# Kernel optimization log

Measured on AMD Instinct MI355X. Metric: run time of the kernel, lower is better.

The kernel has to match this reference:

```python
import jax, jax.numpy as jnp
import numpy as np

B, T, C = 4, 2048, 1024
H = 16
D = C // H  # 64


def setup_inputs() -> dict:
    key = jax.random.key(0)
    ks = jax.random.split(key, 5)
    scale = 0.02
    x = jax.random.normal(ks[0], (B, T, C), dtype=jnp.float32)
    # Linear weights stored in [in, out] layout (equivalent to torch W.T)
    W_qkv = jax.random.normal(ks[1], (C, 3 * C), dtype=jnp.float32) * scale
    b_qkv = jax.random.normal(ks[2], (3 * C,), dtype=jnp.float32) * scale
    W_out = jax.random.normal(ks[3], (C, C), dtype=jnp.float32) * scale
    b_out = jax.random.normal(ks[4], (C,), dtype=jnp.float32) * scale
    return {"x": x, "W_qkv": W_qkv, "b_qkv": b_qkv, "W_out": W_out, "b_out": b_out}


def reference(x, W_qkv, b_qkv, W_out, b_out):
    Bx, Tx, Cx = x.shape
    qkv = x @ W_qkv + b_qkv                      # [B,T,3C]
    qkv = qkv.reshape(Bx, Tx, 3, H, D)
    q = jnp.transpose(qkv[:, :, 0], (0, 2, 1, 3))  # [B,H,T,D]
    k = jnp.transpose(qkv[:, :, 1], (0, 2, 1, 3))
    v = jnp.transpose(qkv[:, :, 2], (0, 2, 1, 3))
    scores = jnp.einsum('bhqd,bhkd->bhqk', q, k) / jnp.sqrt(jnp.float32(D))
    causal = jnp.tril(jnp.ones((Tx, Tx), dtype=bool))  # keep lower triangle
    scores = jnp.where(causal, scores, jnp.float32(-jnp.inf))
    w = jax.nn.softmax(scores, axis=-1)           # dropout p=0.0 (eval)
    out = jnp.einsum('bhqk,bhkd->bhqd', w, v)     # [B,H,T,D]
    out = jnp.transpose(out, (0, 2, 1, 3)).reshape(Bx, Tx, Cx)
    return out @ W_out + b_out
```

## Files before the change

kernel.cpp:

```cpp
#include <hip/hip_runtime.h>

typedef _Float16 f16;
typedef _Float16 f16x4 __attribute__((ext_vector_type(4)));
typedef _Float16 f16x8 __attribute__((ext_vector_type(8)));
typedef float    f32x4 __attribute__((ext_vector_type(4)));

#define B_ 4
#define T_ 2048
#define C_ 1024
#define H_ 16
#define D_ 64

__device__ __forceinline__ void gload_lds16(const f16* g, f16* l) {
  __builtin_amdgcn_global_load_lds(
      (const __attribute__((address_space(1))) unsigned int*)g,
      (__attribute__((address_space(3))) unsigned int*)l, 16, 0, 0);
}

__global__ void cvt_kernel(const float* __restrict__ in, f16* __restrict__ out, int n4) {
  int i = blockIdx.x * blockDim.x + threadIdx.x;
  int stride = gridDim.x * blockDim.x;
  for (; i < n4; i += stride) {
    float4 v = ((const float4*)in)[i];
    f16x4 h = { (f16)v.x, (f16)v.y, (f16)v.z, (f16)v.w };
    ((f16x4*)out)[i] = h;
  }
}

__global__ void transpose_cvt_kernel(const float* __restrict__ W, f16* __restrict__ Wt,
                                     int K, int N) {
  __shared__ f16 tile[32][33];
  int bx = blockIdx.x, by = blockIdx.y;
  int tx = threadIdx.x & 31, ty = threadIdx.x >> 5;
  #pragma unroll
  for (int i = ty; i < 32; i += 8)
    tile[i][tx] = (f16)W[(size_t)(by * 32 + i) * N + bx * 32 + tx];
  __syncthreads();
  #pragma unroll
  for (int i = ty; i < 32; i += 8)
    Wt[(size_t)(bx * 32 + i) * K + by * 32 + tx] = tile[tx][i];
}

template <int EPI>
__global__ __launch_bounds__(256, 3)
void gemm_kernel(const f16* __restrict__ A, const f16* __restrict__ Bt,
                 const float* __restrict__ bias, float* __restrict__ outF,
                 f16* __restrict__ q, f16* __restrict__ kk, f16* __restrict__ vt,
                 int M, int N, int K) {
  __shared__ __align__(16) f16 As[3][128 * 32];
  __shared__ __align__(16) f16 Bs[3][128 * 32];
  const int nbn = N >> 7;
  const int bid = blockIdx.x;
  const int bm = bid / nbn, bn = bid % nbn;
  const int m0 = bm << 7, n0 = bn << 7;
  const int tid = threadIdx.x;
  const int lane = tid & 63, wid = tid >> 6;
  const int wr = wid >> 1, wc = wid & 1;

  f32x4 acc[4][4] = {};

  const int srow = lane >> 2;
  const int scol = (((lane & 3) ^ ((lane >> 2) & 3)) << 3);
  const f16* Abase = A + (size_t)(m0 + srow) * K + scol;
  const f16* Bbase = Bt + (size_t)(n0 + srow) * K + scol;

  auto stage = [&](int buf, int kt) {
    const int c0 = wid * 2;
    #pragma unroll
    for (int c = c0; c < c0 + 2; ++c) {
      gload_lds16(Abase + (size_t)c * 16 * K + kt * 32, &As[buf][c * 512]);
      gload_lds16(Bbase + (size_t)c * 16 * K + kt * 32, &Bs[buf][c * 512]);
    }
  };

  const int g = lane >> 4;
  const int rr = lane & 15;
  const int swz = (g ^ (rr & 3)) << 4;

  auto compute = [&](int buf) {
    f16x8 af[4], bf[4];
    #pragma unroll
    for (int t = 0; t < 4; ++t) {
      af[t] = *(const f16x8*)((const char*)&As[buf][0] + (wr * 64 + t * 16 + rr) * 64 + swz);
      bf[t] = *(const f16x8*)((const char*)&Bs[buf][0] + (wc * 64 + t * 16 + rr) * 64 + swz);
    }
    __builtin_amdgcn_s_setprio(1);
    #pragma unroll
    for (int i = 0; i < 4; ++i)
      #pragma unroll
      for (int j = 0; j < 4; ++j)
        acc[i][j] = __builtin_amdgcn_mfma_f32_16x16x32_f16(af[i], bf[j], acc[i][j], 0, 0, 0);
    __builtin_amdgcn_s_setprio(0);
  };

  const int nk = K >> 5;
  int bcur = 0, bnext = 1, bnn = 2;
  stage(0, 0);
  stage(1, 1);
  asm volatile("s_waitcnt vmcnt(4)" ::: "memory");
  __builtin_amdgcn_s_barrier();
  __builtin_amdgcn_sched_barrier(0);
  for (int t = 0; t < nk; ++t) {
    if (t + 2 < nk) stage(bnn, t + 2);
    compute(bcur);
    if (t + 1 < nk) {
      if (t + 2 < nk) asm volatile("s_waitcnt vmcnt(4)" ::: "memory");
      else            asm volatile("s_waitcnt vmcnt(0)" ::: "memory");
      __builtin_amdgcn_s_barrier();
      __builtin_amdgcn_sched_barrier(0);
    }
    const int tmp = bcur; bcur = bnext; bnext = bnn; bnn = tmp;
  }

  const int col = lane & 15;
  const int row4 = (lane >> 4) << 2;
  #pragma unroll
  for (int i = 0; i < 4; ++i) {
    #pragma unroll
    for (int j = 0; j < 4; ++j) {
      const int n = n0 + wc * 64 + j * 16 + col;
      const float bn_ = bias[n];
      #pragma unroll
      for (int r = 0; r < 4; ++r) {
        const int m = m0 + wr * 64 + i * 16 + row4 + r;
        const float v = acc[i][j][r] + bn_;
        if (EPI == 1) {
          outF[(size_t)m * N + n] = v;
        } else {
          const int which = n >> 10;
          const int cc = n & 1023;
          const int h = cc >> 6, d = cc & 63;
          const int b = m >> 11, t = m & 2047;
          const size_t bh = (size_t)b * 16 + h;
          const f16 hv = (f16)v;
          if (which == 0)      q [(bh * T_ + t) * D_ + d] = hv;
          else if (which == 1) kk[(bh * T_ + t) * D_ + d] = hv;
          else                 vt[(bh * D_ + d) * T_ + t] = hv;
        }
      }
    }
  }
}

__global__ __launch_bounds__(512, 1)
void attn_kernel(const f16* __restrict__ Q, const f16* __restrict__ Kg,
                 const f16* __restrict__ Vt, f16* __restrict__ Aout) {
  __shared__ __align__(16) f16 Ks[3][64 * 64];
  __shared__ __align__(16) f16 Vs[3][64 * 64];
  __shared__ __align__(16) f16 Pt[8][32][72];

  const int bid = blockIdx.x;
  const int wgid = (bid & 7) * 32 + (bid >> 3);
  const int bh = wgid >> 2;
  const int pair = wgid & 3;
  const int lane = threadIdx.x & 63, w = threadIdx.x >> 6;
  const int col = lane & 15;
  const int g = lane >> 4;
  const int ko = g << 3;

  const f16* Qp = Q + (size_t)bh * T_ * D_;
  const f16* Kp = Kg + (size_t)bh * T_ * D_;
  const f16* Vp = Vt + (size_t)bh * D_ * T_;

  const int srow8 = lane >> 3;
  const int scb = ((lane & 7) << 4) ^ (srow8 << 4);
  const int krow_s = (w << 3) + srow8;

  auto stage = [&](int buf, int kb) {
    gload_lds16(Kp + (size_t)(kb + krow_s) * D_ + (scb >> 1), &Ks[buf][w * 512]);
    gload_lds16(Vp + (size_t)krow_s * T_ + kb + (scb >> 1), &Vs[buf][w * 512]);
  };
  auto ldsK = [&](int buf, int krow, int d0) -> f16x8 {
    const int off = krow * 128 + ((d0 << 1) ^ ((krow & 7) << 4));
    return *(const f16x8*)((const char*)&Ks[buf][0] + off);
  };
  auto ldsV = [&](int buf, int drow, int k0) -> f16x8 {
    const int off = drow * 128 + ((k0 << 1) ^ ((drow & 7) << 4));
    return *(const f16x8*)((const char*)&Vs[buf][0] + off);
  };

  const int b = bh >> 4, hd = bh & 15;

  #pragma unroll 1
  for (int tt = 0; tt < 2; ++tt) {
    const int ti = tt ? (7 - pair) : pair;
    const int q0 = ti << 8;
    const int qrow0 = q0 + (w << 5);
    const int nkt = (ti + 1) << 2;

    f16x8 qf[2][2];
    #pragma unroll
    for (int h = 0; h < 2; ++h)
      #pragma unroll
      for (int s = 0; s < 2; ++s) {
        f16x8 t = *(const f16x8*)&Qp[(size_t)(qrow0 + h * 16 + col) * D_ + s * 32 + ko];
        #pragma unroll
        for (int e = 0; e < 8; ++e) t[e] = t[e] * (f16)0.125f;
        qf[h][s] = t;
      }

    f32x4 o[2][4] = {};
    float m[2] = {-1e30f, -1e30f}, l[2] = {0.f, 0.f};

    int b0 = 0, b1 = 1, b2 = 2;
    stage(b0, 0);
    stage(b1, 64);
    asm volatile("s_waitcnt vmcnt(2)" ::: "memory");
    __builtin_amdgcn_s_barrier();
    __builtin_amdgcn_sched_barrier(0);

    for (int kt = 0; kt < nkt; ++kt) {
      const int kb = kt << 6;
      if (kt + 2 < nkt) stage(b2, kb + 128);

      if (kb <= qrow0 + 31) {
        f32x4 sc[2][4] = {};
        #pragma unroll
        for (int s = 0; s < 2; ++s)
          #pragma unroll
          for (int mt = 0; mt < 4; ++mt) {
            f16x8 kf = ldsK(b0, mt * 16 + col, s * 32 + ko);
            sc[0][mt] = __builtin_amdgcn_mfma_f32_16x16x32_f16(kf, qf[0][s], sc[0][mt], 0, 0, 0);
            sc[1][mt] = __builtin_amdgcn_mfma_f32_16x16x32_f16(kf, qf[1][s], sc[1][mt], 0, 0, 0);
          }

        if (kb + 63 > qrow0) {
          #pragma unroll
          for (int mt = 0; mt < 4; ++mt)
            #pragma unroll
            for (int r = 0; r < 4; ++r) {
              const int kv = kb + mt * 16 + (g << 2) + r;
              if (kv > qrow0 + col)      sc[0][mt][r] = -1e30f;
              if (kv > qrow0 + 16 + col) sc[1][mt][r] = -1e30f;
            }
        }

        float mx[2];
        #pragma unroll
        for (int h = 0; h < 2; ++h) {
          float v = fmaxf(fmaxf(fmaxf(sc[h][0][0], sc[h][0][1]), fmaxf(sc[h][0][2], sc[h][0][3])),
                          fmaxf(fmaxf(sc[h][1][0], sc[h][1][1]), fmaxf(sc[h][1][2], sc[h][1][3])));
          v = fmaxf(v, fmaxf(fmaxf(fmaxf(sc[h][2][0], sc[h][2][1]), fmaxf(sc[h][2][2], sc[h][2][3])),
                             fmaxf(fmaxf(sc[h][3][0], sc[h][3][1]), fmaxf(sc[h][3][2], sc[h][3][3]))));
          v = fmaxf(v, __shfl_xor(v, 16, 64));
          v = fmaxf(v, __shfl_xor(v, 32, 64));
          mx[h] = v;
        }

        if (!__all(fmaxf(mx[0] - m[0], mx[1] - m[1]) <= 8.f)) {
          #pragma unroll
          for (int h = 0; h < 2; ++h) {
            const float mnew = fmaxf(m[h], mx[h]);
            const float alpha = __expf(m[h] - mnew);
            m[h] = mnew;
            l[h] *= alpha;
            #pragma unroll
            for (int mt = 0; mt < 4; ++mt)
              #pragma unroll
              for (int r = 0; r < 4; ++r) o[h][mt][r] *= alpha;
          }
        }

        #pragma unroll
        for (int h = 0; h < 2; ++h) {
          float rs = 0.f;
          #pragma unroll
          for (int mt = 0; mt < 4; ++mt) {
            f16x4 ph;
            #pragma unroll
            for (int r = 0; r < 4; ++r) {
              const float p = __expf(sc[h][mt][r] - m[h]);
              rs += p;
              ph[r] = (f16)p;
            }
            *(f16x4*)&Pt[w][h * 16 + col][mt * 16 + (g << 2)] = ph;
          }
          rs += __shfl_xor(rs, 16, 64);
          rs += __shfl_xor(rs, 32, 64);
          l[h] += rs;
        }

        #pragma unroll
        for (int s = 0; s < 2; ++s) {
          f16x8 pb0 = *(const f16x8*)&Pt[w][col][s * 32 + ko];
          f16x8 pb1 = *(const f16x8*)&Pt[w][16 + col][s * 32 + ko];
          #pragma unroll
          for (int mt = 0; mt < 4; ++mt) {
            f16x8 vf = ldsV(b0, mt * 16 + col, s * 32 + ko);
            o[0][mt] = __builtin_amdgcn_mfma_f32_16x16x32_f16(vf, pb0, o[0][mt], 0, 0, 0);
            o[1][mt] = __builtin_amdgcn_mfma_f32_16x16x32_f16(vf, pb1, o[1][mt], 0, 0, 0);
          }
        }
      }

      __builtin_amdgcn_sched_barrier(0);
      if (kt + 2 < nkt) asm volatile("s_waitcnt vmcnt(2)" ::: "memory");
      else              asm volatile("s_waitcnt vmcnt(0)" ::: "memory");
      __builtin_amdgcn_s_barrier();
      __builtin_amdgcn_sched_barrier(0);
      const int tmp = b0; b0 = b1; b1 = b2; b2 = tmp;
    }

    #pragma unroll
    for (int h = 0; h < 2; ++h) {
      const float inv = 1.0f / l[h];
      const int t = qrow0 + h * 16 + col;
      const size_t rowoff = ((size_t)b * T_ + t) * C_ + (size_t)hd * D_;
      #pragma unroll
      for (int mt = 0; mt < 4; ++mt) {
        f16x4 ov;
        #pragma unroll
        for (int r = 0; r < 4; ++r) ov[r] = (f16)(o[h][mt][r] * inv);
        *(f16x4*)&Aout[rowoff + mt * 16 + (g << 2)] = ov;
      }
    }
    __builtin_amdgcn_s_barrier();
  }
}

extern "C" void kernel_launch(void* const* d_in, const int* in_sizes, int n_in,
                              void* d_out, int out_size, void* d_ws, size_t ws_size,
                              hipStream_t stream) {
  const float* x    = (const float*)d_in[0];
  const float* Wqkv = (const float*)d_in[1];
  const float* bqkv = (const float*)d_in[2];
  const float* Wout = (const float*)d_in[3];
  const float* bout = (const float*)d_in[4];
  float* out = (float*)d_out;

  char* ws = (char*)d_ws;
  f16* xb     = (f16*)ws;
  f16* Wqkv_t = (f16*)(ws + (16u << 20));
  f16* Wout_t = (f16*)(ws + (22u << 20));
  f16* Qb     = (f16*)(ws + (24u << 20));
  f16* Kb     = (f16*)(ws + (40u << 20));
  f16* Vtb    = (f16*)(ws + (56u << 20));

  cvt_kernel<<<2048, 256, 0, stream>>>(x, xb, (B_ * T_ * C_) / 4);
  dim3 g1(3072 / 32, 1024 / 32);
  transpose_cvt_kernel<<<g1, 256, 0, stream>>>(Wqkv, Wqkv_t, 1024, 3072);
  dim3 g2(1024 / 32, 1024 / 32);
  transpose_cvt_kernel<<<g2, 256, 0, stream>>>(Wout, Wout_t, 1024, 1024);

  gemm_kernel<0><<<64 * 24, 256, 0, stream>>>(xb, Wqkv_t, bqkv, nullptr,
                                              Qb, Kb, Vtb, 8192, 3072, 1024);
  attn_kernel<<<256, 512, 0, stream>>>(Qb, Kb, Vtb, xb );
  gemm_kernel<1><<<64 * 8, 256, 0, stream>>>(xb, Wout_t, bout, out,
                                             nullptr, nullptr, nullptr, 8192, 1024, 1024);
}
```

Before: 213.1 us.

## Shrink attention workgroups to 4 waves and process two KV tiles per barrier

The attention kernel now runs 512 workgroups of 256 threads (two per CU) covering 128 query rows each, down from 256 workgroups of 512 threads covering 256 rows. Each loop iteration computes two 64-key tiles between barriers, using a four-buffer K/V ring filled two tiles ahead. The P scratch buffer switches to an XOR-swizzled layout to avoid LDS bank conflicts. The intent is higher occupancy and half as many barriers per key tile. The cost is that each K/V tile is loaded by twice as many workgroups, and vmcnt(0) waits may expose load latency.

```diff
diff --git a/kernel.cpp b/kernel.cpp
--- a/kernel.cpp
+++ b/kernel.cpp
@@ -142,17 +142,17 @@
   }
 }
 
-__global__ __launch_bounds__(512, 1)
+__global__ __launch_bounds__(256, 2)
 void attn_kernel(const f16* __restrict__ Q, const f16* __restrict__ Kg,
                  const f16* __restrict__ Vt, f16* __restrict__ Aout) {
-  __shared__ __align__(16) f16 Ks[3][64 * 64];
-  __shared__ __align__(16) f16 Vs[3][64 * 64];
-  __shared__ __align__(16) f16 Pt[8][32][72];
+  __shared__ __align__(16) f16 Ks[4][64 * 64];
+  __shared__ __align__(16) f16 Vs[4][64 * 64];
+  __shared__ __align__(16) f16 Pt[4][32 * 64];
 
   const int bid = blockIdx.x;
-  const int wgid = (bid & 7) * 32 + (bid >> 3);
-  const int bh = wgid >> 2;
-  const int pair = wgid & 3;
+  const int wgid = (bid & 7) * 64 + (bid >> 3);
+  const int bh = wgid >> 3;
+  const int pr = wgid & 7;
   const int lane = threadIdx.x & 63, w = threadIdx.x >> 6;
   const int col = lane & 15;
   const int g = lane >> 4;
@@ -162,13 +162,16 @@
   const f16* Kp = Kg + (size_t)bh * T_ * D_;
   const f16* Vp = Vt + (size_t)bh * D_ * T_;
 
-  const int srow8 = lane >> 3;
-  const int scb = ((lane & 7) << 4) ^ (srow8 << 4);
-  const int krow_s = (w << 3) + srow8;
+  const int sr = lane >> 3;
+  const int sc = ((lane & 7) ^ (sr & 7)) << 3;
 
   auto stage = [&](int buf, int kb) {
-    gload_lds16(Kp + (size_t)(kb + krow_s) * D_ + (scb >> 1), &Ks[buf][w * 512]);
-    gload_lds16(Vp + (size_t)krow_s * T_ + kb + (scb >> 1), &Vs[buf][w * 512]);
+    #pragma unroll
+    for (int c2 = 0; c2 < 2; ++c2) {
+      const int c = (w << 1) + c2;
+      gload_lds16(Kp + (size_t)(kb + (c << 3) + sr) * D_ + sc, &Ks[buf][c * 512]);
+      gload_lds16(Vp + (size_t)((c << 3) + sr) * T_ + kb + sc, &Vs[buf][c * 512]);
+    }
   };
   auto ldsK = [&](int buf, int krow, int d0) -> f16x8 {
     const int off = krow * 128 + ((d0 << 1) ^ ((krow & 7) << 4));
@@ -179,14 +182,14 @@
     return *(const f16x8*)((const char*)&Vs[buf][0] + off);
   };
 
+  char* PtW = (char*)&Pt[w][0];
   const int b = bh >> 4, hd = bh & 15;
 
   #pragma unroll 1
   for (int tt = 0; tt < 2; ++tt) {
-    const int ti = tt ? (7 - pair) : pair;
-    const int q0 = ti << 8;
-    const int qrow0 = q0 + (w << 5);
-    const int nkt = (ti + 1) << 2;
+    const int ti = tt ? (15 - pr) : pr;
+    const int qrow0 = (ti << 7) + (w << 5);
+    const int np = ti + 1;
 
     f16x8 qf[2][2];
     #pragma unroll
@@ -202,103 +205,108 @@
     f32x4 o[2][4] = {};
     float m[2] = {-1e30f, -1e30f}, l[2] = {0.f, 0.f};
 
-    int b0 = 0, b1 = 1, b2 = 2;
-    stage(b0, 0);
-    stage(b1, 64);
-    asm volatile("s_waitcnt vmcnt(2)" ::: "memory");
-    __builtin_amdgcn_s_barrier();
-    __builtin_amdgcn_sched_barrier(0);
-
-    for (int kt = 0; kt < nkt; ++kt) {
-      const int kb = kt << 6;
-      if (kt + 2 < nkt) stage(b2, kb + 128);
-
-      if (kb <= qrow0 + 31) {
-        f32x4 sc[2][4] = {};
-        #pragma unroll
-        for (int s = 0; s < 2; ++s)
+    auto COMPUTE = [&](int buf, int kb) {
+      f32x4 sc2[2][4] = {};
+      #pragma unroll
+      for (int s = 0; s < 2; ++s)
+        #pragma unroll
+        for (int mt = 0; mt < 4; ++mt) {
+          f16x8 kf = ldsK(buf, mt * 16 + col, s * 32 + ko);
+          sc2[0][mt] = __builtin_amdgcn_mfma_f32_16x16x32_f16(kf, qf[0][s], sc2[0][mt], 0, 0, 0);
+          sc2[1][mt] = __builtin_amdgcn_mfma_f32_16x16x32_f16(kf, qf[1][s], sc2[1][mt], 0, 0, 0);
+        }
+
+      if (kb + 63 > qrow0) {
+        #pragma unroll
+        for (int mt = 0; mt < 4; ++mt)
           #pragma unroll
-          for (int mt = 0; mt < 4; ++mt) {
-            f16x8 kf = ldsK(b0, mt * 16 + col, s * 32 + ko);
-            sc[0][mt] = __builtin_amdgcn_mfma_f32_16x16x32_f16(kf, qf[0][s], sc[0][mt], 0, 0, 0);
-            sc[1][mt] = __builtin_amdgcn_mfma_f32_16x16x32_f16(kf, qf[1][s], sc[1][mt], 0, 0, 0);
+          for (int r = 0; r < 4; ++r) {
+            const int kv = kb + mt * 16 + (g << 2) + r;
+            if (kv > qrow0 + col)      sc2[0][mt][r] = -1e30f;
+            if (kv > qrow0 + 16 + col) sc2[1][mt][r] = -1e30f;
           }
-
-        if (kb + 63 > qrow0) {
+      }
+
+      float mx[2];
+      #pragma unroll
+      for (int h = 0; h < 2; ++h) {
+        float v = fmaxf(fmaxf(fmaxf(sc2[h][0][0], sc2[h][0][1]), fmaxf(sc2[h][0][2], sc2[h][0][3])),
+                        fmaxf(fmaxf(sc2[h][1][0], sc2[h][1][1]), fmaxf(sc2[h][1][2], sc2[h][1][3])));
+        v = fmaxf(v, fmaxf(fmaxf(fmaxf(sc2[h][2][0], sc2[h][2][1]), fmaxf(sc2[h][2][2], sc2[h][2][3])),
+                           fmaxf(fmaxf(sc2[h][3][0], sc2[h][3][1]), fmaxf(sc2[h][3][2], sc2[h][3][3]))));
+        v = fmaxf(v, __shfl_xor(v, 16, 64));
+        v = fmaxf(v, __shfl_xor(v, 32, 64));
+        mx[h] = v;
+      }
+
+      if (!__all(fmaxf(mx[0] - m[0], mx[1] - m[1]) <= 8.f)) {
+        #pragma unroll
+        for (int h = 0; h < 2; ++h) {
+          const float mnew = fmaxf(m[h], mx[h]);
+          const float alpha = __expf(m[h] - mnew);
+          m[h] = mnew;
+          l[h] *= alpha;
           #pragma unroll
           for (int mt = 0; mt < 4; ++mt)
             #pragma unroll
-            for (int r = 0; r < 4; ++r) {
-              const int kv = kb + mt * 16 + (g << 2) + r;
-              if (kv > qrow0 + col)      sc[0][mt][r] = -1e30f;
-              if (kv > qrow0 + 16 + col) sc[1][mt][r] = -1e30f;
-            }
-        }
-
-        float mx[2];
-        #pragma unroll
-        for (int h = 0; h < 2; ++h) {
-          float v = fmaxf(fmaxf(fmaxf(sc[h][0][0], sc[h][0][1]), fmaxf(sc[h][0][2], sc[h][0][3])),
-                          fmaxf(fmaxf(sc[h][1][0], sc[h][1][1]), fmaxf(sc[h][1][2], sc[h][1][3])));
-          v = fmaxf(v, fmaxf(fmaxf(fmaxf(sc[h][2][0], sc[h][2][1]), fmaxf(sc[h][2][2], sc[h][2][3])),
-                             fmaxf(fmaxf(sc[h][3][0], sc[h][3][1]), fmaxf(sc[h][3][2], sc[h][3][3]))));
-          v = fmaxf(v, __shfl_xor(v, 16, 64));
-          v = fmaxf(v, __shfl_xor(v, 32, 64));
-          mx[h] = v;
-        }
-
-        if (!__all(fmaxf(mx[0] - m[0], mx[1] - m[1]) <= 8.f)) {
+            for (int r = 0; r < 4; ++r) o[h][mt][r] *= alpha;
+        }
+      }
+
+      #pragma unroll
+      for (int h = 0; h < 2; ++h) {
+        float rs = 0.f;
+        #pragma unroll
+        for (int mt = 0; mt < 4; ++mt) {
+          f16x4 ph;
           #pragma unroll
-          for (int h = 0; h < 2; ++h) {
-            const float mnew = fmaxf(m[h], mx[h]);
-            const float alpha = __expf(m[h] - mnew);
-            m[h] = mnew;
-            l[h] *= alpha;
-            #pragma unroll
-            for (int mt = 0; mt < 4; ++mt)
-              #pragma unroll
-              for (int r = 0; r < 4; ++r) o[h][mt][r] *= alpha;
+          for (int r = 0; r < 4; ++r) {
+            const float p = __expf(sc2[h][mt][r] - m[h]);
+            rs += p;
+            ph[r] = (f16)p;
           }
-        }
-
-        #pragma unroll
-        for (int h = 0; h < 2; ++h) {
-          float rs = 0.f;
-          #pragma unroll
-          for (int mt = 0; mt < 4; ++mt) {
-            f16x4 ph;
-            #pragma unroll
-            for (int r = 0; r < 4; ++r) {
-              const float p = __expf(sc[h][mt][r] - m[h]);
-              rs += p;
-              ph[r] = (f16)p;
-            }
-            *(f16x4*)&Pt[w][h * 16 + col][mt * 16 + (g << 2)] = ph;
-          }
-          rs += __shfl_xor(rs, 16, 64);
-          rs += __shfl_xor(rs, 32, 64);
-          l[h] += rs;
-        }
-
-        #pragma unroll
-        for (int s = 0; s < 2; ++s) {
-          f16x8 pb0 = *(const f16x8*)&Pt[w][col][s * 32 + ko];
-          f16x8 pb1 = *(const f16x8*)&Pt[w][16 + col][s * 32 + ko];
-          #pragma unroll
-          for (int mt = 0; mt < 4; ++mt) {
-            f16x8 vf = ldsV(b0, mt * 16 + col, s * 32 + ko);
-            o[0][mt] = __builtin_amdgcn_mfma_f32_16x16x32_f16(vf, pb0, o[0][mt], 0, 0, 0);
-            o[1][mt] = __builtin_amdgcn_mfma_f32_16x16x32_f16(vf, pb1, o[1][mt], 0, 0, 0);
-          }
-        }
-      }
+          *(f16x4*)(PtW + (h * 16 + col) * 128 + (((mt << 5) + (g << 3)) ^ ((col & 7) << 4))) = ph;
+        }
+        rs += __shfl_xor(rs, 16, 64);
+        rs += __shfl_xor(rs, 32, 64);
+        l[h] += rs;
+      }
+
+      #pragma unroll
+      for (int s = 0; s < 2; ++s) {
+        const int pcb = ((s << 6) + (g << 4)) ^ ((col & 7) << 4);
+        f16x8 pb0 = *(const f16x8*)(PtW + col * 128 + pcb);
+        f16x8 pb1 = *(const f16x8*)(PtW + (16 + col) * 128 + pcb);
+        #pragma unroll
+        for (int mt = 0; mt < 4; ++mt) {
+          f16x8 vf = ldsV(buf, mt * 16 + col, s * 32 + ko);
+          o[0][mt] = __builtin_amdgcn_mfma_f32_16x16x32_f16(vf, pb0, o[0][mt], 0, 0, 0);
+          o[1][mt] = __builtin_amdgcn_mfma_f32_16x16x32_f16(vf, pb1, o[1][mt], 0, 0, 0);
+        }
+      }
+    };
+
+    stage(0, 0);
+    stage(1, 64);
+    asm volatile("s_waitcnt vmcnt(0)" ::: "memory");
+    __builtin_amdgcn_s_barrier();
+    __builtin_amdgcn_sched_barrier(0);
+
+    #pragma unroll 1
+    for (int j = 0; j < np; ++j) {
+      const int kb0 = j << 7;
+      const int s0 = (j << 1) & 3, s1 = ((j << 1) + 1) & 3;
+      if (j + 1 < np) {
+        stage((s0 + 2) & 3, kb0 + 128);
+        stage((s1 + 2) & 3, kb0 + 192);
+      }
+      COMPUTE(s0, kb0);
+      if (kb0 + 64 <= qrow0 + 31) COMPUTE(s1, kb0 + 64);
 
       __builtin_amdgcn_sched_barrier(0);
-      if (kt + 2 < nkt) asm volatile("s_waitcnt vmcnt(2)" ::: "memory");
-      else              asm volatile("s_waitcnt vmcnt(0)" ::: "memory");
+      asm volatile("s_waitcnt vmcnt(0)" ::: "memory");
       __builtin_amdgcn_s_barrier();
       __builtin_amdgcn_sched_barrier(0);
-      const int tmp = b0; b0 = b1; b1 = b2; b2 = tmp;
     }
 
     #pragma unroll
@@ -344,7 +352,7 @@
 
   gemm_kernel<0><<<64 * 24, 256, 0, stream>>>(xb, Wqkv_t, bqkv, nullptr,
                                               Qb, Kb, Vtb, 8192, 3072, 1024);
-  attn_kernel<<<256, 512, 0, stream>>>(Qb, Kb, Vtb, xb );
+  attn_kernel<<<512, 256, 0, stream>>>(Qb, Kb, Vtb, xb );
   gemm_kernel<1><<<64 * 8, 256, 0, stream>>>(xb, Wout_t, bout, out,
                                              nullptr, nullptr, nullptr, 8192, 1024, 1024);
 }
```

Measured after the change: 207.9 us. 1.02x faster.
